# Optimization experiments

Measured on AMD Instinct MI355X. Metric: run time of the kernel, lower is better.

Reference implementation:

```python
import jax, jax.numpy as jnp
import numpy as np

B_, G_, H_ = 16, 4096, 128
D_INNER, D_STATE, NHEADS, HEADDIM, CHUNK, D_CONV = 256, 16, 4, 64, 64, 4
LATENT = 64
D_IN_PROJ = 2 * D_INNER + 2 * D_STATE + NHEADS  # 548
CONV_DIM = D_INNER + 2 * D_STATE                # 288
NLAYERS = 4  # [fwd0, fwd1, bwd0, bwd1]
EPS = 1e-5


def _segsum(x):
    # x: (..., T) -> (..., T, T) stable segment sums, -inf above diagonal
    T = x.shape[-1]
    xe = jnp.broadcast_to(x[..., None], x.shape + (T,))
    lo = jnp.tril(jnp.ones((T, T), bool), -1)
    s = jnp.cumsum(jnp.where(lo, xe, 0.0), axis=-2)
    keep = jnp.tril(jnp.ones((T, T), bool), 0)
    return jnp.where(keep, s, -jnp.inf)


def _ssd(x, A, B, C):
    # x: (b, L, h, p), A: (b, L, h), B/C: (b, L, n)  (single shared head for B/C)
    b, L, h, p = x.shape
    c = L // CHUNK
    x = x.reshape(b, c, CHUNK, h, p)
    A = A.reshape(b, c, CHUNK, h).transpose(0, 3, 1, 2)  # b h c l
    B = B.reshape(b, c, CHUNK, -1)                       # b c l n
    C = C.reshape(b, c, CHUNK, -1)
    A_cs = jnp.cumsum(A, axis=-1)
    Lmat = jnp.exp(_segsum(A))                           # b h c l s
    Y_diag = jnp.einsum('bcln,bcsn,bhcls,bcshp->bclhp', C, B, Lmat, x)
    decay_states = jnp.exp(A_cs[:, :, :, -1:] - A_cs)
    states = jnp.einsum('bcln,bhcl,bclhp->bchpn', B, decay_states, x)
    states = jnp.concatenate([jnp.zeros_like(states[:, :1]), states], axis=1)
    decay_chunk = jnp.exp(_segsum(jnp.pad(A_cs[:, :, :, -1], ((0, 0), (0, 0), (1, 0)))))
    new_states = jnp.einsum('bhzc,bchpn->bzhpn', decay_chunk, states)
    states = new_states[:, :-1]
    sdo = jnp.exp(A_cs)
    Y_off = jnp.einsum('bcln,bchpn,bhcl->bclhp', C, states, sdo)
    return (Y_diag + Y_off).reshape(b, L, h, p)


def _mamba2(u, Wi, cw, cb, dtb, Alog, Dp, nw, Wo):
    b, L, _ = u.shape
    zxbcdt = u @ Wi.T                                   # (b, L, 548)
    z = zxbcdt[..., :D_INNER]
    xBC = zxbcdt[..., D_INNER:D_INNER + CONV_DIM]
    dt = jax.nn.softplus(zxbcdt[..., D_INNER + CONV_DIM:] + dtb)  # (b, L, h)
    # depthwise causal conv1d, padding=d_conv-1, keep first L outputs
    xt = xBC.transpose(0, 2, 1)
    y = jax.lax.conv_general_dilated(xt, cw[:, None, :], (1,), [(D_CONV - 1, D_CONV - 1)],
                                     dimension_numbers=('NCH', 'OIH', 'NCH'),
                                     feature_group_count=CONV_DIM)
    xBC = jax.nn.silu((y[:, :, :L] + cb[None, :, None]).transpose(0, 2, 1))
    x = xBC[..., :D_INNER].reshape(b, L, NHEADS, HEADDIM)
    Bm = xBC[..., D_INNER:D_INNER + D_STATE]
    Cm = xBC[..., D_INNER + D_STATE:]
    A = -jnp.exp(Alog)                                  # (h,)
    yssd = _ssd(x * dt[..., None], A * dt, Bm, Cm)
    yssd = yssd + x * Dp[:, None]
    yf = yssd.reshape(b, L, D_INNER)
    yf = yf * jax.nn.silu(z)                            # gated RMSNorm
    yf = yf * jax.lax.rsqrt(jnp.mean(yf * yf, -1, keepdims=True) + EPS) * nw
    return yf @ Wo.T


def _forward(expression, noise, expr_w, expr_b, in_proj_w, conv_w, conv_b, dt_bias,
             A_log, D_par, norm_w, out_proj_w, fusion_w, fusion_b, lm_w, lm_b,
             lv_w, lv_b, gate_w, gate_b, outp_w, outp_b, reg_gate):
    x = expression[..., None] * expr_w[:, 0] + expr_b   # Linear(1, H) -> (b, G, H)
    fwd = x
    for i in (0, 1):
        fwd = _mamba2(fwd, in_proj_w[i], conv_w[i], conv_b[i], dt_bias[i],
                      A_log[i], D_par[i], norm_w[i], out_proj_w[i])
    bwd = x[:, ::-1]
    for i in (2, 3):
        bwd = _mamba2(bwd, in_proj_w[i], conv_w[i], conv_b[i], dt_bias[i],
                      A_log[i], D_par[i], norm_w[i], out_proj_w[i])
    bwd = bwd[:, ::-1]
    fused = jax.nn.gelu(jnp.concatenate([fwd, bwd], -1) @ fusion_w.T + fusion_b,
                        approximate=False)
    lm = fused @ lm_w.T + lm_b
    lv = fused @ lv_w.T + lv_b
    sample = lm + noise * jnp.exp(0.5 * lv)             # reparameterize
    gate = jax.nn.sigmoid(sample @ gate_w.T + gate_b)
    h = fused * gate
    pred = (h @ outp_w.T + outp_b)[..., 0] * jax.nn.sigmoid(reg_gate)
    return pred, lm, lv, sample


def setup_inputs() -> dict:
    key = jax.random.key(0)
    ks = jax.random.split(key, 24)
    def w(k, shape, s=0.02):
        return jax.random.normal(k, shape, jnp.float32) * s
    return dict(
        expression=jax.random.uniform(ks[0], (B_, G_), jnp.float32),
        noise=jax.random.normal(ks[1], (B_, G_, LATENT), jnp.float32),
        expr_w=w(ks[2], (H_, 1), 0.2), expr_b=w(ks[3], (H_,)),
        in_proj_w=w(ks[4], (NLAYERS, D_IN_PROJ, H_)),
        conv_w=w(ks[5], (NLAYERS, CONV_DIM, D_CONV), 0.1),
        conv_b=w(ks[6], (NLAYERS, CONV_DIM)),
        dt_bias=jax.random.uniform(ks[7], (NLAYERS, NHEADS), jnp.float32, -4.0, 1.0),
        A_log=jnp.full((NLAYERS, NHEADS), -jnp.log(2.0), jnp.float32),
        D_par=jnp.ones((NLAYERS, NHEADS), jnp.float32),
        norm_w=jnp.ones((NLAYERS, D_INNER), jnp.float32),
        out_proj_w=w(ks[8], (NLAYERS, H_, D_INNER)),
        fusion_w=w(ks[9], (H_, 2 * H_)), fusion_b=w(ks[10], (H_,)),
        lm_w=w(ks[11], (LATENT, H_)), lm_b=w(ks[12], (LATENT,)),
        lv_w=w(ks[13], (LATENT, H_)), lv_b=w(ks[14], (LATENT,)),
        gate_w=w(ks[15], (H_, LATENT)), gate_b=w(ks[16], (H_,)),
        outp_w=w(ks[17], (1, H_)), outp_b=w(ks[18], (1,)),
        reg_gate=w(ks[19], (G_,), 0.01),
    )


def reference(expression, noise, expr_w, expr_b, in_proj_w, conv_w, conv_b, dt_bias,
              A_log, D_par, norm_w, out_proj_w, fusion_w, fusion_b, lm_w, lm_b,
              lv_w, lv_b, gate_w, gate_b, outp_w, outp_b, reg_gate):
    return _forward(expression, noise, expr_w, expr_b, in_proj_w, conv_w, conv_b,
                    dt_bias, A_log, D_par, norm_w, out_proj_w, fusion_w, fusion_b,
                    lm_w, lm_b, lv_w, lv_b, gate_w, gate_b, outp_w, outp_b, reg_gate)
```

## Files before the change

### kernel.cpp

```cpp
#include <hip/hip_runtime.h>
#include <math.h>

#define HMOD 128
#define DIN 256
#define NHEADS 4
#define HD 64
#define DSTATE 16
#define NCH 64
#define CONVD 288
#define DPROJ 548
#define LAT 64
#define LSEQ 4096

typedef __attribute__((ext_vector_type(8))) short bf16x8;
typedef __attribute__((ext_vector_type(4))) float f32x4;
typedef __attribute__((ext_vector_type(8))) unsigned short u16x8;

__device__ __forceinline__ float sigm(float x){ return 1.0f/(1.0f+__expf(-x)); }
__device__ __forceinline__ float siluf(float x){ return x/(1.0f+__expf(-x)); }
__device__ __forceinline__ float softplusf(float x){ return (x>20.0f)? x : log1pf(expf(x)); }
__device__ __forceinline__ float geluf(float x){ return 0.5f*x*(1.0f+erff(x*0.70710678118654752440f)); }
__device__ __forceinline__ unsigned short f2bf(float x){
  unsigned int u = __float_as_uint(x);
  return (unsigned short)((u + 0x7FFFu + ((u>>16)&1u)) >> 16);
}
__device__ __forceinline__ float bf2f(unsigned short h){
  return __uint_as_float(((unsigned int)h)<<16);
}

__global__ __launch_bounds__(256) void cvt_kernel(const float* __restrict__ in,
  unsigned short* __restrict__ out, int n)
{
  int i = blockIdx.x*256 + threadIdx.x;
  if (i < n) out[i] = f2bf(in[i]);
}
__global__ __launch_bounds__(256) void cvt_nw_kernel(const float* __restrict__ in,
  const float* __restrict__ nw, unsigned short* __restrict__ out, int n)
{
  int i = blockIdx.x*256 + threadIdx.x;
  if (i < n){
    int k = i & 255;
    int li = i >> 15;
    out[i] = f2bf(in[i]*nw[li*256 + k]);
  }
}
__global__ __launch_bounds__(256) void cvt_cw_kernel(const float* __restrict__ in,
  float* __restrict__ out)
{
  int i = blockIdx.x*256 + threadIdx.x;
  if (i < 4608){
    int li = i/1152, r = i - li*1152;
    int ch = r>>2, k = r&3;
    out[li*1152 + k*CONVD + ch] = in[i];
  }
}

__global__ __launch_bounds__(256) void embed_kernel(const float* __restrict__ expr,
    const float* __restrict__ ew, const float* __restrict__ eb,
    unsigned short* __restrict__ actA, unsigned short* __restrict__ actB)
{
  int gid = blockIdx.x*256 + threadIdx.x;
  int m = gid >> 7, hh = gid & 127;
  int bl = m >> 12, g = m & 4095;
  unsigned short v = f2bf(expr[m]*ew[hh] + eb[hh]);
  actA[gid] = v;
  actB[(size_t)(((bl<<12) | (4095-g))<<7) + hh] = v;
}

template<int KDIM, int NT, int EPI>
__global__ __launch_bounds__(256) void gemm3(
    const unsigned short* __restrict__ A,
    const unsigned short* __restrict__ A2,
    const unsigned short* __restrict__ Wb,
    const float* __restrict__ bias,
    const float* __restrict__ bias2,
    const float* __restrict__ ssqp,
    unsigned short* __restrict__ ob1,
    unsigned short* __restrict__ ob2,
    float* __restrict__ of1,
    float* __restrict__ of2,
    int N, int ldc)
{
  __shared__ unsigned short Ws[64*(KDIM+8)];
  __shared__ unsigned short Cb[(EPI==5) ? 8 : 128*72];
  const int tid = threadIdx.x;
  const int m0 = blockIdx.x<<7;
  const int wid = tid>>6, lane = tid&63;
  const int la = lane&15, kq = lane>>4;
  const int mw = m0 + wid*32;

  bf16x8 af[KDIM/32][2];
  #pragma unroll
  for (int ki=0; ki<KDIM/32; ki++){
    int k = ki*32 + kq*8;
    #pragma unroll
    for (int mf=0; mf<2; mf++){
      int row = mw + mf*16 + la;
      const unsigned short* src;
      if (EPI==2){
        if (k < 128) src = A + (size_t)row*128 + k;
        else { int bl2=row>>12, t=row&4095; src = A2 + (size_t)(((bl2<<12)|(4095-t)))*128 + (k-128); }
      } else {
        src = A + (size_t)row*KDIM + k;
      }
      af[ki][mf] = *(const bf16x8*)src;
    }
  }
  float scv[2][4];
  if (EPI==4){
    #pragma unroll
    for (int mf=0; mf<2; mf++)
      #pragma unroll
      for (int r=0; r<4; r++){
        int m = mw + mf*16 + kq*4 + r;
        float s = ssqp[m*4]+ssqp[m*4+1]+ssqp[m*4+2]+ssqp[m*4+3];
        scv[mf][r] = rsqrtf(s*(1.0f/256.0f) + 1e-5f);
      }
  }

  const int KD8 = KDIM/8;
  for (int nt=0; nt<NT; nt++){
    int n0 = (blockIdx.y*NT + nt)<<6;
    for (int ci = tid; ci < 64*KD8; ci += 256){
      int row = ci/KD8, kc = (ci - row*KD8)*8;
      int n = n0 + row;
      bf16x8 v = {0,0,0,0,0,0,0,0};
      if (n < N) v = *(const bf16x8*)&Wb[(size_t)n*KDIM + kc];
      *(bf16x8*)&Ws[row*(KDIM+8) + kc] = v;
    }
    __syncthreads();
    f32x4 acc[2][4] = {};
    #pragma unroll
    for (int ki=0; ki<KDIM/32; ki++){
      #pragma unroll
      for (int nf=0; nf<4; nf++){
        bf16x8 bfr = *(const bf16x8*)&Ws[(nf*16 + la)*(KDIM+8) + ki*32 + kq*8];
        #pragma unroll
        for (int mf=0; mf<2; mf++)
          acc[mf][nf] = __builtin_amdgcn_mfma_f32_16x16x32_bf16(af[ki][mf], bfr, acc[mf][nf], 0,0,0);
      }
    }
    #pragma unroll
    for (int mf=0; mf<2; mf++){
      #pragma unroll
      for (int nf=0; nf<4; nf++){
        #pragma unroll
        for (int r=0; r<4; r++){
          int m = mw + mf*16 + kq*4 + r;
          int row = wid*32 + mf*16 + kq*4 + r;
          int n = n0 + nf*16 + la;
          int col = nf*16 + la;
          float v = acc[mf][nf][r];
          if (EPI==1){
            if (n >= DIN+CONVD && n < DPROJ)
              of1[(size_t)m*NHEADS + (n-DIN-CONVD)] = softplusf(v + bias[n-DIN-CONVD]);
            else
              Cb[row*72 + col] = f2bf(v);
          } else if (EPI==2){
            Cb[row*72 + col] = f2bf(geluf(v + bias[n]));
          } else if (EPI==4){
            Cb[row*72 + col] = f2bf(v*scv[mf][r]);
          } else if (EPI==5){
            float* dst = (n < 64) ? of1 : of2;
            float b = (n < 64) ? bias[n] : bias2[n-64];
            dst[(size_t)m*64 + (n&63)] = v + b;
          }
        }
      }
    }
    if (EPI!=5){
      __syncthreads();
      #pragma unroll
      for (int j=0; j<4; j++){
        int row = (tid>>3) + j*32;
        int col0 = (tid&7)*8;
        int m = m0 + row;
        int nch = n0 + col0;
        u16x8 val = *(const u16x8*)&Cb[row*72 + col0];
        if (EPI==1){
          if (nch < DIN)            *(u16x8*)&ob1[(size_t)m*DIN + nch] = val;
          else if (nch < DIN+CONVD) *(u16x8*)&ob2[(size_t)m*CONVD + (nch-DIN)] = val;
        } else {
          *(u16x8*)&ob1[(size_t)m*ldc + nch] = val;
        }
      }
    }
    __syncthreads();
  }
}

__global__ __launch_bounds__(256) void conv_kernel(const unsigned short* __restrict__ xraw,
  const float* __restrict__ cwT, const float* __restrict__ cb,
  unsigned short* __restrict__ xconv)
{
  int gid = blockIdx.x*256 + threadIdx.x;
  int m = gid / 36, v = gid - (gid/36)*36;
  int ch0 = v*8;
  int t = m & 4095;
  float acc[8];
  float4 b0 = *(const float4*)&cb[ch0];
  float4 b1 = *(const float4*)&cb[ch0+4];
  acc[0]=b0.x; acc[1]=b0.y; acc[2]=b0.z; acc[3]=b0.w;
  acc[4]=b1.x; acc[5]=b1.y; acc[6]=b1.z; acc[7]=b1.w;
  #pragma unroll
  for (int k=0;k<4;k++){
    int tt = t - 3 + k;
    if (tt >= 0){
      u16x8 xv = *(const u16x8*)&xraw[(size_t)(m-3+k)*CONVD + ch0];
      float4 w0 = *(const float4*)&cwT[k*CONVD + ch0];
      float4 w1 = *(const float4*)&cwT[k*CONVD + ch0 + 4];
      float w[8] = {w0.x,w0.y,w0.z,w0.w,w1.x,w1.y,w1.z,w1.w};
      #pragma unroll
      for (int j=0;j<8;j++) acc[j] = fmaf(w[j], bf2f(xv[j]), acc[j]);
    }
  }
  u16x8 o;
  #pragma unroll
  for (int j=0;j<8;j++) o[j] = f2bf(siluf(acc[j]));
  *(u16x8*)&xconv[(size_t)m*CONVD + ch0] = o;
}

__global__ __launch_bounds__(256) void ssd_front(
  const unsigned short* __restrict__ xconv, const float* __restrict__ dtsp,
  const float* __restrict__ Alog,
  float* __restrict__ states_g, float* __restrict__ acs_g, float* __restrict__ atot_g)
{
  __shared__ __align__(16) unsigned short Xt[64*88];
  __shared__ __align__(16) unsigned short Raw[64*72];
  __shared__ __align__(16) unsigned short Braw[64*24];
  __shared__ __align__(16) unsigned short Bwt[16*88];
  __shared__ float acs_s[64], dts_s[64];
  const int bx = blockIdx.x;
  const int h = bx & 3, c = (bx>>2)&63, bl = bx>>8;
  const int tid = threadIdx.x;
  const int tokbase = (bl<<12) + (c<<6);

  if (tid < 64) {
    float dt = dtsp[(size_t)(tokbase+tid)*NHEADS + h];
    dts_s[tid] = dt;
    float xsc = -__expf(Alog[h]) * dt;
    #pragma unroll
    for (int off=1; off<64; off<<=1){ float v = __shfl_up(xsc, off); if (tid >= off) xsc += v; }
    acs_s[tid] = xsc;
    acs_g[(size_t)bx*64 + tid] = xsc;
  }
  #pragma unroll
  for (int i=0;i<2;i++){
    int idx = tid + (i<<8);
    int l = idx>>3, g = idx&7;
    *(u16x8*)&Raw[l*72 + g*8] = *(const u16x8*)&xconv[(size_t)(tokbase+l)*CONVD + h*64 + g*8];
  }
  if (tid < 128){
    int l = tid>>1, half = tid&1;
    *(u16x8*)&Braw[l*24 + half*8] = *(const u16x8*)&xconv[(size_t)(tokbase+l)*CONVD + 256 + half*8];
  }
  __syncthreads();
  const float atotv = acs_s[63];
  if (tid==0) atot_g[bx] = atotv;
  #pragma unroll
  for (int i=0;i<2;i++){
    int u = tid + (i<<8);
    int ch = u & 63, l0 = (u>>6)*8;
    u16x8 o;
    #pragma unroll
    for (int j=0;j<8;j++) o[j] = Raw[(l0+j)*72 + ch];
    *(u16x8*)&Xt[ch*88 + l0] = o;
  }
  if (tid < 128){
    int ch = tid & 15, l0 = (tid>>4)*8;
    u16x8 o;
    #pragma unroll
    for (int j=0;j<8;j++){
      int l = l0+j;
      o[j] = f2bf(bf2f(Braw[l*24 + ch]) * __expf(atotv - acs_s[l]) * dts_s[l]);
    }
    *(u16x8*)&Bwt[ch*88 + l0] = o;
  }
  __syncthreads();
  const int wid = tid>>6, lane = tid&63;
  const int la = lane&15, kq = lane>>4;
  f32x4 acc = {0.f,0.f,0.f,0.f};
  #pragma unroll
  for (int kt=0; kt<2; kt++){
    bf16x8 a = *(const bf16x8*)&Xt[(wid*16+la)*88 + kt*32+kq*8];
    bf16x8 b = *(const bf16x8*)&Bwt[la*88 + kt*32+kq*8];
    acc = __builtin_amdgcn_mfma_f32_16x16x32_bf16(a, b, acc, 0,0,0);
  }
  size_t base = (size_t)bx<<10;
  #pragma unroll
  for (int r=0;r<4;r++){
    int p = wid*16 + kq*4 + r;
    states_g[base + (size_t)p*16 + la] = acc[r];
  }
}

__global__ __launch_bounds__(256) void scan_kernel(float* __restrict__ states,
  const float* __restrict__ atot)
{
  int gid = blockIdx.x*256 + threadIdx.x;
  int inner = gid & 1023;
  int h = (gid>>10)&3;
  int bl = gid>>12;
  size_t base = (size_t)bl*262144 + h*1024 + inner;
  int abase = bl*256 + h;
  float v[64];
  #pragma unroll
  for (int c2=0;c2<64;c2++) v[c2] = states[base + (size_t)c2*4096];
  float S = 0.0f;
  #pragma unroll
  for (int c2=0;c2<64;c2++){
    states[base + (size_t)c2*4096] = S;
    S = __expf(atot[abase + c2*4])*S + v[c2];
  }
}

__global__ __launch_bounds__(256) void ssd_back(
  const unsigned short* __restrict__ xconv, const unsigned short* __restrict__ zb,
  const float* __restrict__ dtsp, const float* __restrict__ acs_g,
  const float* __restrict__ states, const float* __restrict__ Dp,
  unsigned short* __restrict__ yf, float* __restrict__ ssqp)
{
  __shared__ __align__(16) unsigned short Xt[64*88];
  __shared__ __align__(16) unsigned short SbRaw[64*88];
  __shared__ __align__(16) unsigned short CBS[3*64*56];
  __shared__ float acs_s[64], dts_s[64];
  unsigned short* Cp = CBS;
  unsigned short* Bp = CBS + 64*56;
  unsigned short* Sp = CBS + 2*64*56;
  float* Yl = (float*)CBS;
  const int bx = blockIdx.x;
  const int h = bx & 3, c = (bx>>2)&63, bl = bx>>8;
  const int tid = threadIdx.x;
  const int tokbase = (bl<<12) + (c<<6);

  if (tid < 64) {
    dts_s[tid] = dtsp[(size_t)(tokbase+tid)*NHEADS + h];
    acs_s[tid] = acs_g[(size_t)bx*64 + tid];
  }
  for (int i = tid; i < 1024; i += 256){
    int l = i>>4, k = 16 + (i&15);
    Cp[l*56+k] = 0; Bp[l*56+k] = 0; Sp[l*56+k] = 0;
  }
  #pragma unroll
  for (int i=0;i<2;i++){
    int idx = tid + (i<<8);
    int l = idx>>3, g = idx&7;
    *(u16x8*)&SbRaw[l*88 + g*8] = *(const u16x8*)&xconv[(size_t)(tokbase+l)*CONVD + h*64 + g*8];
  }
  {
    int l = tid>>2, part = tid&3;
    u16x8 vv = *(const u16x8*)&xconv[(size_t)(tokbase+l)*CONVD + 256 + part*8];
    if (part < 2) *(u16x8*)&Bp[l*56 + part*8] = vv;
    else          *(u16x8*)&Cp[l*56 + (part-2)*8] = vv;
  }
  #pragma unroll
  for (int i=0;i<4;i++){
    int e = tid + (i<<8);
    int p = e>>4, n = e&15;
    Sp[p*56+n] = f2bf(states[((size_t)bx<<10) + e]);
  }
  __syncthreads();
  #pragma unroll
  for (int i=0;i<2;i++){
    int u = tid + (i<<8);
    int ch = u & 63, l0 = (u>>6)*8;
    u16x8 o;
    #pragma unroll
    for (int j=0;j<8;j++) o[j] = SbRaw[(l0+j)*88 + ch];
    *(u16x8*)&Xt[ch*88 + l0] = o;
  }
  __syncthreads();

  const int wid = tid>>6, lane = tid&63;
  const int la = lane&15, kq = lane>>4;
  const int L0 = wid*16;
  const f32x4 zero4 = {0.f,0.f,0.f,0.f};
  const float Dh = Dp[h];
  unsigned short* Sb = SbRaw;

  {
    bf16x8 a = *(const bf16x8*)&Cp[(L0+la)*56 + kq*8];
    f32x4 cbacc[4];
    #pragma unroll
    for (int nf=0; nf<4; nf++){
      bf16x8 b = *(const bf16x8*)&Bp[(nf*16+la)*56 + kq*8];
      cbacc[nf] = __builtin_amdgcn_mfma_f32_16x16x32_bf16(a, b, zero4, 0,0,0);
    }
    #pragma unroll
    for (int nf=0; nf<4; nf++){
      #pragma unroll
      for (int r=0; r<4; r++){
        int l = L0 + kq*4 + r, s = nf*16 + la;
        float v = 0.f;
        if (s <= l) v = __expf(acs_s[l]-acs_s[s])*dts_s[s]*cbacc[nf][r];
        if (s == l) v += Dh;
        Sb[l*88 + s] = f2bf(v);
      }
    }
  }
  f32x4 ya[4];
  {
    bf16x8 a = *(const bf16x8*)&Cp[(L0+la)*56 + kq*8];
    #pragma unroll
    for (int nf=0; nf<4; nf++){
      bf16x8 b = *(const bf16x8*)&Sp[(nf*16+la)*56 + kq*8];
      ya[nf] = __builtin_amdgcn_mfma_f32_16x16x32_bf16(a, b, zero4, 0,0,0);
    }
    float eal[4];
    #pragma unroll
    for (int r=0; r<4; r++) eal[r] = __expf(acs_s[L0 + kq*4 + r]);
    #pragma unroll
    for (int nf=0; nf<4; nf++)
      #pragma unroll
      for (int r=0; r<4; r++) ya[nf][r] *= eal[r];
  }
  #pragma unroll
  for (int kt=0; kt<2; kt++){
    bf16x8 a = *(const bf16x8*)&Sb[(L0+la)*88 + kt*32+kq*8];
    #pragma unroll
    for (int nf=0; nf<4; nf++){
      bf16x8 b = *(const bf16x8*)&Xt[(nf*16+la)*88 + kt*32+kq*8];
      ya[nf] = __builtin_amdgcn_mfma_f32_16x16x32_bf16(a, b, ya[nf], 0,0,0);
    }
  }
  __syncthreads();
  #pragma unroll
  for (int nf=0; nf<4; nf++){
    #pragma unroll
    for (int r=0; r<4; r++){
      int l = L0 + kq*4 + r, p = nf*16 + la;
      Yl[l*76 + p] = ya[nf][r];
    }
  }
  __syncthreads();
  #pragma unroll
  for (int i=0;i<2;i++){
    int u = tid + (i<<8);
    int l = u>>3, g = u&7;
    size_t gidx = (size_t)(tokbase+l)*DIN + (h<<6) + g*8;
    u16x8 z8 = *(const u16x8*)&zb[gidx];
    u16x8 o8;
    float ps = 0.f;
    #pragma unroll
    for (int j=0;j<8;j++){
      float y = Yl[l*76 + g*8 + j];
      float zv = bf2f(z8[j]);
      float yv = y * zv * sigm(zv);
      o8[j] = f2bf(yv);
      ps = fmaf(yv, yv, ps);
    }
    *(u16x8*)&yf[gidx] = o8;
    ps += __shfl_xor(ps, 1); ps += __shfl_xor(ps, 2); ps += __shfl_xor(ps, 4);
    if (g == 0) ssqp[(size_t)(tokbase+l)*NHEADS + h] = ps;
  }
}

__global__ __launch_bounds__(256) void sample_kernel(const float* __restrict__ lm,
  const float* __restrict__ lv, const float* __restrict__ nz, float* __restrict__ sp)
{
  int gid = blockIdx.x*256 + threadIdx.x;
  sp[gid] = fmaf(nz[gid], expf(0.5f*lv[gid]), lm[gid]);
}

__global__ __launch_bounds__(256) void gatepred_kernel(
  const unsigned short* __restrict__ fused, const float* __restrict__ sample,
  const float* __restrict__ gw, const float* __restrict__ gb,
  const float* __restrict__ ow, const float* __restrict__ ob,
  const float* __restrict__ rg, float* __restrict__ pred)
{
  __shared__ float gws[128][65];
  __shared__ float gbs[128], ows[128];
  const int tid = threadIdx.x;
  #pragma unroll
  for (int i=0;i<32;i++){ int e = tid + (i<<8); gws[e>>6][e&63] = gw[e]; }
  if (tid < 128){ gbs[tid] = gb[tid]; ows[tid] = ow[tid]; }
  __syncthreads();
  const int wave = tid>>6, lane = tid&63;
  const float ob0 = ob[0];
  for (int it=0; it<16; it++){
    int m = blockIdx.x*64 + wave*16 + it;
    float sv = sample[(size_t)m*LAT + lane];
    float acc0 = gbs[lane], acc1 = gbs[lane+64];
    #pragma unroll
    for (int k=0;k<64;k++){
      float sk = __shfl(sv, k);
      acc0 = fmaf(sk, gws[lane][k], acc0);
      acc1 = fmaf(sk, gws[lane+64][k], acc1);
    }
    float f0 = bf2f(fused[(size_t)m*128 + lane]);
    float f1 = bf2f(fused[(size_t)m*128 + 64 + lane]);
    float cval = f0*sigm(acc0)*ows[lane] + f1*sigm(acc1)*ows[lane+64];
    #pragma unroll
    for (int off=32; off; off>>=1) cval += __shfl_xor(cval, off);
    if (lane==0) pred[m] = (cval + ob0) * sigm(rg[m & 4095]);
  }
}

extern "C" void kernel_launch(void* const* d_in, const int* in_sizes, int n_in,
                              void* d_out, int out_size, void* d_ws, size_t ws_size,
                              hipStream_t stream)
{
  const float* expr      = (const float*)d_in[0];
  const float* noise     = (const float*)d_in[1];
  const float* expr_w    = (const float*)d_in[2];
  const float* expr_b    = (const float*)d_in[3];
  const float* in_proj_w = (const float*)d_in[4];
  const float* conv_w    = (const float*)d_in[5];
  const float* conv_b    = (const float*)d_in[6];
  const float* dt_bias   = (const float*)d_in[7];
  const float* A_log     = (const float*)d_in[8];
  const float* D_par     = (const float*)d_in[9];
  const float* norm_w    = (const float*)d_in[10];
  const float* out_proj_w= (const float*)d_in[11];
  const float* fusion_w  = (const float*)d_in[12];
  const float* fusion_b  = (const float*)d_in[13];
  const float* lm_w      = (const float*)d_in[14];
  const float* lm_b      = (const float*)d_in[15];
  const float* lv_w      = (const float*)d_in[16];
  const float* lv_b      = (const float*)d_in[17];
  const float* gate_w    = (const float*)d_in[18];
  const float* gate_b    = (const float*)d_in[19];
  const float* outp_w    = (const float*)d_in[20];
  const float* outp_b    = (const float*)d_in[21];
  const float* reg_gate  = (const float*)d_in[22];

  const size_t WBYTES = 940032;
  int BG = 0;
  const int cands[5] = {16, 8, 4, 2, 1};
  for (int ci = 0; ci < 5; ci++) {
    int c2 = cands[ci];
    size_t MGc = (size_t)c2 * LSEQ;
    size_t need = WBYTES + MGc*2992 + (size_t)c2*1024 + 256;
    if (need <= ws_size) { BG = c2; break; }
  }
  if (!BG) return;
  const size_t MG = (size_t)BG * LSEQ;

  unsigned short* wip = (unsigned short*)d_ws;
  unsigned short* wop = wip + 280576;
  unsigned short* wfu = wop + 131072;
  unsigned short* wlm = wfu + 32768;
  unsigned short* wlv = wlm + 8192;
  float* cwT   = (float*)(wlv + 8192);
  float* dtsp  = (float*)((char*)d_ws + WBYTES);
  float* acs   = dtsp + MG*4;
  float* atot  = acs  + MG*4;
  float* states= atot + (size_t)BG*256;
  float* ssqp  = states + MG*64;
  unsigned short* zb    = (unsigned short*)(ssqp + MG*4);
  unsigned short* xrawb = zb    + MG*256;
  unsigned short* xcv   = xrawb + MG*288;
  unsigned short* actA  = xcv   + MG*288;
  unsigned short* actB  = actA  + MG*128;
  unsigned short* yfb   = actB  + MG*128;
  unsigned short* fusedbf = yfb;

  float* out_pred_g = (float*)d_out;
  float* out_lm_g   = out_pred_g + (size_t)16*LSEQ;
  float* out_lv_g   = out_lm_g   + (size_t)16*LSEQ*LAT;
  float* out_samp_g = out_lv_g   + (size_t)16*LSEQ*LAT;

  cvt_kernel<<<(280576+255)/256, 256, 0, stream>>>(in_proj_w, wip, 280576);
  cvt_nw_kernel<<<131072/256,    256, 0, stream>>>(out_proj_w, norm_w, wop, 131072);
  cvt_kernel<<<32768/256,        256, 0, stream>>>(fusion_w, wfu, 32768);
  cvt_kernel<<<8192/256,         256, 0, stream>>>(lm_w, wlm, 8192);
  cvt_kernel<<<8192/256,         256, 0, stream>>>(lv_w, wlv, 8192);
  cvt_cw_kernel<<<(4608+255)/256, 256, 0, stream>>>(conv_w, cwT);

  for (int b0 = 0; b0 < 16; b0 += BG) {
    float* out_pred = out_pred_g + (size_t)b0*LSEQ;
    float* out_lm   = out_lm_g   + (size_t)b0*LSEQ*LAT;
    float* out_lv   = out_lv_g   + (size_t)b0*LSEQ*LAT;
    float* out_samp = out_samp_g + (size_t)b0*LSEQ*LAT;
    const float* nz = noise      + (size_t)b0*LSEQ*LAT;

    embed_kernel<<<(MG*128)/256, 256, 0, stream>>>(expr + (size_t)b0*LSEQ, expr_w, expr_b, actA, actB);

    for (int li = 0; li < 4; li++) {
      unsigned short* u = (li < 2) ? actA : actB;
      const unsigned short* Wi = wip + (size_t)li*DPROJ*HMOD;
      const unsigned short* Wo = wop + (size_t)li*HMOD*DIN;
      const float* cwTl = cwT + (size_t)li*1152;
      const float* cb   = conv_b + (size_t)li*CONVD;
      const float* dtb  = dt_bias + (size_t)li*NHEADS;
      const float* Al   = A_log + (size_t)li*NHEADS;
      const float* Dl   = D_par + (size_t)li*NHEADS;

      gemm3<128,3,1><<<dim3(MG/128, 3), 256, 0, stream>>>(u, nullptr, Wi, dtb, nullptr, nullptr, zb, xrawb, dtsp, nullptr, DPROJ, 0);
      conv_kernel<<<(MG*36)/256, 256, 0, stream>>>(xrawb, cwTl, cb, xcv);
      ssd_front<<<BG*256, 256, 0, stream>>>(xcv, dtsp, Al, states, acs, atot);
      scan_kernel<<<(BG*LSEQ)/256, 256, 0, stream>>>(states, atot);
      ssd_back<<<BG*256, 256, 0, stream>>>(xcv, zb, dtsp, acs, states, Dl, yfb, ssqp);
      gemm3<256,2,4><<<dim3(MG/128, 1), 256, 0, stream>>>(yfb, nullptr, Wo, nullptr, nullptr, ssqp, u, nullptr, nullptr, nullptr, HMOD, HMOD);
    }

    gemm3<256,2,2><<<dim3(MG/128, 1), 256, 0, stream>>>(actA, actB, wfu, fusion_b, nullptr, nullptr, fusedbf, nullptr, nullptr, nullptr, HMOD, HMOD);
    gemm3<128,2,5><<<dim3(MG/128, 1), 256, 0, stream>>>(fusedbf, nullptr, wlm, lm_b, lv_b, nullptr, nullptr, nullptr, out_lm, out_lv, 128, LAT);
    sample_kernel<<<(MG*LAT)/256, 256, 0, stream>>>(out_lm, out_lv, nz, out_samp);
    gatepred_kernel<<<MG/64, 256, 0, stream>>>(fusedbf, out_samp, gate_w, gate_b, outp_w, outp_b, reg_gate, out_pred);
  }
}
```

Baseline: 659.5 us.

## Fuse sampling into latent GEMM epilogue, MFMA gate kernel, single-pass in_proj

The reparameterised sample is now computed in the lm/lv GEMM epilogue, which keeps the lm values in registers and drops the separate sample kernel and its reloads. The scalar gate/pred kernel is replaced by an MFMA bf16 version that converts the sample to bf16 and reduces against fused activations through LDS. The in_proj GEMM now loops over all 9 N-tiles in one block instead of using a 3-wide grid, so the A fragments are loaded once but there is less parallelism. Computing the gate in bf16 adds precision risk.

```diff
diff --git a/kernel.cpp b/kernel.cpp
--- a/kernel.cpp
+++ b/kernel.cpp
@@ -79,6 +79,8 @@
     unsigned short* __restrict__ ob2,
     float* __restrict__ of1,
     float* __restrict__ of2,
+    const float* __restrict__ nzp,
+    float* __restrict__ of3,
     int N, int ldc)
 {
   __shared__ unsigned short Ws[64*(KDIM+8)];
@@ -117,6 +119,7 @@
         scv[mf][r] = rsqrtf(s*(1.0f/256.0f) + 1e-5f);
       }
   }
+  float vlm[2][4][4];
 
   const int KD8 = KDIM/8;
   for (int nt=0; nt<NT; nt++){
@@ -161,9 +164,16 @@
           } else if (EPI==4){
             Cb[row*72 + col] = f2bf(v*scv[mf][r]);
           } else if (EPI==5){
-            float* dst = (n < 64) ? of1 : of2;
-            float b = (n < 64) ? bias[n] : bias2[n-64];
-            dst[(size_t)m*64 + (n&63)] = v + b;
+            if (nt == 0){
+              float lm = v + bias[col];
+              vlm[mf][nf][r] = lm;
+              of1[(size_t)m*64 + col] = lm;
+            } else {
+              float lv = v + bias2[col];
+              of2[(size_t)m*64 + col] = lv;
+              float nzv = nzp[(size_t)m*64 + col];
+              of3[(size_t)m*64 + col] = fmaf(nzv, expf(0.5f*lv), vlm[mf][nf][r]);
+            }
           }
         }
       }
@@ -455,44 +465,91 @@
   }
 }
 
-__global__ __launch_bounds__(256) void sample_kernel(const float* __restrict__ lm,
-  const float* __restrict__ lv, const float* __restrict__ nz, float* __restrict__ sp)
-{
-  int gid = blockIdx.x*256 + threadIdx.x;
-  sp[gid] = fmaf(nz[gid], expf(0.5f*lv[gid]), lm[gid]);
-}
-
-__global__ __launch_bounds__(256) void gatepred_kernel(
+__global__ __launch_bounds__(256) void predgate_kernel(
   const unsigned short* __restrict__ fused, const float* __restrict__ sample,
-  const float* __restrict__ gw, const float* __restrict__ gb,
+  const unsigned short* __restrict__ gwb, const float* __restrict__ gb,
   const float* __restrict__ ow, const float* __restrict__ ob,
   const float* __restrict__ rg, float* __restrict__ pred)
 {
-  __shared__ float gws[128][65];
-  __shared__ float gbs[128], ows[128];
+  __shared__ __align__(16) unsigned short Ws[64*72];
+  __shared__ __align__(16) float Gp[128*68];
   const int tid = threadIdx.x;
-  #pragma unroll
-  for (int i=0;i<32;i++){ int e = tid + (i<<8); gws[e>>6][e&63] = gw[e]; }
-  if (tid < 128){ gbs[tid] = gb[tid]; ows[tid] = ow[tid]; }
-  __syncthreads();
-  const int wave = tid>>6, lane = tid&63;
+  const int m0 = blockIdx.x<<7;
+  const int wid = tid>>6, lane = tid&63;
+  const int la = lane&15, kq = lane>>4;
+  const int mw = m0 + wid*32;
+
+  bf16x8 af[2][2];
+  #pragma unroll
+  for (int ki=0; ki<2; ki++){
+    int k = ki*32 + kq*8;
+    #pragma unroll
+    for (int mf=0; mf<2; mf++){
+      int row = mw + mf*16 + la;
+      float4 s0 = *(const float4*)&sample[(size_t)row*64 + k];
+      float4 s1 = *(const float4*)&sample[(size_t)row*64 + k + 4];
+      bf16x8 o;
+      o[0]=(short)f2bf(s0.x); o[1]=(short)f2bf(s0.y); o[2]=(short)f2bf(s0.z); o[3]=(short)f2bf(s0.w);
+      o[4]=(short)f2bf(s1.x); o[5]=(short)f2bf(s1.y); o[6]=(short)f2bf(s1.z); o[7]=(short)f2bf(s1.w);
+      af[ki][mf] = o;
+    }
+  }
   const float ob0 = ob[0];
-  for (int it=0; it<16; it++){
-    int m = blockIdx.x*64 + wave*16 + it;
-    float sv = sample[(size_t)m*LAT + lane];
-    float acc0 = gbs[lane], acc1 = gbs[lane+64];
-    #pragma unroll
-    for (int k=0;k<64;k++){
-      float sk = __shfl(sv, k);
-      acc0 = fmaf(sk, gws[lane][k], acc0);
-      acc1 = fmaf(sk, gws[lane+64][k], acc1);
-    }
-    float f0 = bf2f(fused[(size_t)m*128 + lane]);
-    float f1 = bf2f(fused[(size_t)m*128 + 64 + lane]);
-    float cval = f0*sigm(acc0)*ows[lane] + f1*sigm(acc1)*ows[lane+64];
-    #pragma unroll
-    for (int off=32; off; off>>=1) cval += __shfl_xor(cval, off);
-    if (lane==0) pred[m] = (cval + ob0) * sigm(rg[m & 4095]);
+  const int prow = tid>>1, phalf = tid&1;
+  float rs = 0.f;
+
+  #pragma unroll
+  for (int nt=0; nt<2; nt++){
+    int n0 = nt<<6;
+    #pragma unroll
+    for (int i=0;i<2;i++){
+      int slot = tid + (i<<8);
+      int row = slot>>3, g = slot&7;
+      *(u16x8*)&Ws[row*72 + g*8] = *(const u16x8*)&gwb[(size_t)(n0+row)*64 + g*8];
+    }
+    __syncthreads();
+    f32x4 acc[2][4] = {};
+    #pragma unroll
+    for (int ki=0; ki<2; ki++){
+      #pragma unroll
+      for (int nf=0; nf<4; nf++){
+        bf16x8 bfr = *(const bf16x8*)&Ws[(nf*16 + la)*72 + ki*32 + kq*8];
+        #pragma unroll
+        for (int mf=0; mf<2; mf++)
+          acc[mf][nf] = __builtin_amdgcn_mfma_f32_16x16x32_bf16(af[ki][mf], bfr, acc[mf][nf], 0,0,0);
+      }
+    }
+    #pragma unroll
+    for (int mf=0; mf<2; mf++){
+      #pragma unroll
+      for (int nf=0; nf<4; nf++){
+        #pragma unroll
+        for (int r=0; r<4; r++){
+          int row = wid*32 + mf*16 + kq*4 + r;
+          int col = nf*16 + la;
+          int n = n0 + col;
+          Gp[row*68 + col] = sigm(acc[mf][nf][r] + gb[n]) * ow[n];
+        }
+      }
+    }
+    __syncthreads();
+    #pragma unroll
+    for (int q=0; q<4; q++){
+      int col0 = phalf*32 + q*8;
+      u16x8 f8 = *(const u16x8*)&fused[(size_t)(m0+prow)*128 + n0 + col0];
+      float4 g0 = *(const float4*)&Gp[prow*68 + col0];
+      float4 g1 = *(const float4*)&Gp[prow*68 + col0 + 4];
+      rs = fmaf(bf2f(f8[0]), g0.x, rs); rs = fmaf(bf2f(f8[1]), g0.y, rs);
+      rs = fmaf(bf2f(f8[2]), g0.z, rs); rs = fmaf(bf2f(f8[3]), g0.w, rs);
+      rs = fmaf(bf2f(f8[4]), g1.x, rs); rs = fmaf(bf2f(f8[5]), g1.y, rs);
+      rs = fmaf(bf2f(f8[6]), g1.z, rs); rs = fmaf(bf2f(f8[7]), g1.w, rs);
+    }
+    __syncthreads();
+  }
+  rs += __shfl_xor(rs, 1);
+  if (phalf == 0){
+    int m = m0 + prow;
+    pred[m] = (rs + ob0) * sigm(rg[m & 4095]);
   }
 }
 
@@ -524,7 +581,7 @@
   const float* outp_b    = (const float*)d_in[21];
   const float* reg_gate  = (const float*)d_in[22];
 
-  const size_t WBYTES = 940032;
+  const size_t WBYTES = 956416;
   int BG = 0;
   const int cands[5] = {16, 8, 4, 2, 1};
   for (int ci = 0; ci < 5; ci++) {
@@ -541,7 +598,8 @@
   unsigned short* wfu = wop + 131072;
   unsigned short* wlm = wfu + 32768;
   unsigned short* wlv = wlm + 8192;
-  float* cwT   = (float*)(wlv + 8192);
+  unsigned short* wgw = wlv + 8192;
+  float* cwT   = (float*)(wgw + 8192);
   float* dtsp  = (float*)((char*)d_ws + WBYTES);
   float* acs   = dtsp + MG*4;
   float* atot  = acs  + MG*4;
@@ -565,6 +623,7 @@
   cvt_kernel<<<32768/256,        256, 0, stream>>>(fusion_w, wfu, 32768);
   cvt_kernel<<<8192/256,         256, 0, stream>>>(lm_w, wlm, 8192);
   cvt_kernel<<<8192/256,         256, 0, stream>>>(lv_w, wlv, 8192);
+  cvt_kernel<<<8192/256,         256, 0, stream>>>(gate_w, wgw, 8192);
   cvt_cw_kernel<<<(4608+255)/256, 256, 0, stream>>>(conv_w, cwT);
 
   for (int b0 = 0; b0 < 16; b0 += BG) {
@@ -586,17 +645,16 @@
       const float* Al   = A_log + (size_t)li*NHEADS;
       const float* Dl   = D_par + (size_t)li*NHEADS;
 
-      gemm3<128,3,1><<<dim3(MG/128, 3), 256, 0, stream>>>(u, nullptr, Wi, dtb, nullptr, nullptr, zb, xrawb, dtsp, nullptr, DPROJ, 0);
+      gemm3<128,9,1><<<dim3(MG/128, 1), 256, 0, stream>>>(u, nullptr, Wi, dtb, nullptr, nullptr, zb, xrawb, dtsp, nullptr, nullptr, nullptr, DPROJ, 0);
       conv_kernel<<<(MG*36)/256, 256, 0, stream>>>(xrawb, cwTl, cb, xcv);
       ssd_front<<<BG*256, 256, 0, stream>>>(xcv, dtsp, Al, states, acs, atot);
       scan_kernel<<<(BG*LSEQ)/256, 256, 0, stream>>>(states, atot);
       ssd_back<<<BG*256, 256, 0, stream>>>(xcv, zb, dtsp, acs, states, Dl, yfb, ssqp);
-      gemm3<256,2,4><<<dim3(MG/128, 1), 256, 0, stream>>>(yfb, nullptr, Wo, nullptr, nullptr, ssqp, u, nullptr, nullptr, nullptr, HMOD, HMOD);
-    }
-
-    gemm3<256,2,2><<<dim3(MG/128, 1), 256, 0, stream>>>(actA, actB, wfu, fusion_b, nullptr, nullptr, fusedbf, nullptr, nullptr, nullptr, HMOD, HMOD);
-    gemm3<128,2,5><<<dim3(MG/128, 1), 256, 0, stream>>>(fusedbf, nullptr, wlm, lm_b, lv_b, nullptr, nullptr, nullptr, out_lm, out_lv, 128, LAT);
-    sample_kernel<<<(MG*LAT)/256, 256, 0, stream>>>(out_lm, out_lv, nz, out_samp);
-    gatepred_kernel<<<MG/64, 256, 0, stream>>>(fusedbf, out_samp, gate_w, gate_b, outp_w, outp_b, reg_gate, out_pred);
-  }
-}
+      gemm3<256,2,4><<<dim3(MG/128, 1), 256, 0, stream>>>(yfb, nullptr, Wo, nullptr, nullptr, ssqp, u, nullptr, nullptr, nullptr, nullptr, nullptr, HMOD, HMOD);
+    }
+
+    gemm3<256,2,2><<<dim3(MG/128, 1), 256, 0, stream>>>(actA, actB, wfu, fusion_b, nullptr, nullptr, fusedbf, nullptr, nullptr, nullptr, nullptr, nullptr, HMOD, HMOD);
+    gemm3<128,2,5><<<dim3(MG/128, 1), 256, 0, stream>>>(fusedbf, nullptr, wlm, lm_b, lv_b, nullptr, nullptr, nullptr, out_lm, out_lv, nz, out_samp, 128, LAT);
+    predgate_kernel<<<MG/128, 256, 0, stream>>>(fusedbf, out_samp, wgw, gate_b, outp_w, outp_b, reg_gate, out_pred);
+  }
+}
```

Result: faster. 632.4 us (-4.1%).
